# Optimization experiments

Hardware: AMD Instinct MI355X
Metric: run time of the kernel (lower is better)

The kernel has to match this reference:

```python
import jax, jax.numpy as jnp
import numpy as np

N_NODES = 100000
N_EDGES = 1600000
FEAT = 512
CLS = 64
HID = 200  # each hop layer output width; 3 hops -> 600 concat


def spmm(row, col, vals, x):
    # out[r] = sum_{e: row[e]==r} vals[e] * x[col[e]]  -- sparse A @ x
    return jax.ops.segment_sum(x[col] * vals[:, None], row, num_segments=x.shape[0])


def setup_inputs() -> dict:
    key = jax.random.key(0)
    ks = jax.random.split(key, 12)
    adj_index = jax.random.randint(ks[0], (2, N_EDGES), 0, N_NODES, dtype=jnp.int64)
    # scale like a normalized adjacency (~1/avg_degree) to keep powers stable
    adj_values = jax.random.uniform(ks[1], (N_EDGES,), dtype=jnp.float32) * (1.0 / 16.0)
    features = jax.random.normal(ks[2], (N_NODES, FEAT), dtype=jnp.float32)
    s1 = (2.0 / (FEAT + HID)) ** 0.5
    s2 = (2.0 / (3 * HID + HID)) ** 0.5
    sf = (2.0 / (3 * HID + CLS)) ** 0.5
    W1 = jax.random.normal(ks[3], (3, FEAT, HID), dtype=jnp.float32) * s1
    b1 = jax.random.normal(ks[4], (3, HID), dtype=jnp.float32) * 0.01
    W2 = jax.random.normal(ks[5], (3, 3 * HID, HID), dtype=jnp.float32) * s2
    b2 = jax.random.normal(ks[6], (3, HID), dtype=jnp.float32) * 0.01
    Wfc = jax.random.normal(ks[7], (3 * HID, CLS), dtype=jnp.float32) * sf
    bfc = jax.random.normal(ks[8], (CLS,), dtype=jnp.float32) * 0.01
    return {"adj_index": adj_index, "adj_values": adj_values, "features": features,
            "W1": W1, "b1": b1, "W2": W2, "b2": b2, "Wfc": Wfc, "bfc": bfc}


def reference(adj_index, adj_values, features, W1, b1, W2, b2, Wfc, bfc):
    # Inference mode: dropout is identity.
    row, col = adj_index[0], adj_index[1]
    # upper (sparse) layers: linear + bias + relu, then (iterations-1) spmm hops
    outs1 = []
    for i in range(3):  # iterations = i + 1
        h = jax.nn.relu(features @ W1[i] + b1[i][None, :])
        for _ in range(i):
            h = spmm(row, col, adj_values, h)
        outs1.append(h)
    abstract1 = jnp.concatenate(outs1, axis=1)  # [N, 600]
    # bottom (dense) layers: linear, (iterations-1) spmm hops, then + bias
    outs2 = []
    for i in range(3):
        h = abstract1 @ W2[i]
        for _ in range(i):
            h = spmm(row, col, adj_values, h)
        h = h + b2[i][None, :]
        outs2.append(h)
    abstract2 = jnp.concatenate(outs2, axis=1)  # [N, 600]
    node_emb = abstract2 @ Wfc + bfc  # [N, CLS]
    predictions = jax.nn.log_softmax(node_emb, axis=1)
    return node_emb, predictions
```

## Files before the change

### kernel.cpp

```cpp
#include <hip/hip_runtime.h>

typedef unsigned short u16;
typedef unsigned int u32;
typedef __attribute__((ext_vector_type(8))) short short8;
typedef __attribute__((ext_vector_type(4))) float f32x4;
typedef __attribute__((ext_vector_type(4))) u32 u32x4;
typedef __attribute__((ext_vector_type(2))) u32 u32x2;

#define NN 100000
#define PAD 640

__device__ __forceinline__ float b2f(u16 u) {
    union { u32 i; float f; } v; v.i = ((u32)u) << 16; return v.f;
}
__device__ __forceinline__ u16 f2b(float f) {
    union { float f; u32 i; } v; v.f = f;
    u32 x = v.i;
    return (u16)((x + 0x7FFFu + ((x >> 16) & 1u)) >> 16);
}
__device__ __forceinline__ u32 pack2(float lo, float hi) {
    return (u32)f2b(lo) | ((u32)f2b(hi) << 16);
}
__device__ __forceinline__ float rdf(const void* p, size_t i, int f) {
    return f ? ((const float*)p)[i] : b2f(((const u16*)p)[i]);
}
__device__ __forceinline__ void gload16(const u16* g, u16* l) {
    __builtin_amdgcn_global_load_lds(
        (const __attribute__((address_space(1))) void*)g,
        (__attribute__((address_space(3))) void*)l, 16, 0, 0);
}

__global__ void probe_k(const int* __restrict__ idx,
                        const void* avals, const void* feats, const void* W1,
                        const void* b1, const void* W2, const void* b2,
                        const void* Wfc, const void* bfc,
                        int* __restrict__ flags) {
    if (blockIdx.x != 0 || threadIdx.x >= 64) return;
    int lane = threadIdx.x;
    int v0 = idx[2 * lane + 1];
    int v1 = idx[2 * (lane + 64) + 1];
    int ok = (v0 == 0 && v1 == 0);
    int allz = __all(ok);
    if (lane == 0) flags[0] = allz ? 1 : 0;
    const void* ts[8] = {avals, feats, W1, b1, W2, b2, Wfc, bfc};
    const int ns[8] = {256, 256, 256, 128, 256, 128, 256, 32};
    for (int t = 0; t < 8; ++t) {
        const u16* p = (const u16*)ts[t];
        int n = ns[t], bad = 0;
        for (int i = lane; i < n; i += 64) {
            int e = (p[2 * i] >> 7) & 0xFF;
            if (e >= 133) bad++;
        }
        for (int off = 32; off; off >>= 1) bad += __shfl_xor(bad, off, 64);
        if (lane == 0) flags[1 + t] = (bad * 8 >= n) ? 1 : 0;
    }
}

__device__ __forceinline__ int load_row(const int* idx, int E, int f, int e) {
    return f ? idx[2 * e] : idx[e];
}
__device__ __forceinline__ int load_col(const int* idx, int E, int f, int e) {
    return f ? idx[2 * E + 2 * e] : idx[E + e];
}

__global__ void featconv_k(const void* __restrict__ src, u16* __restrict__ dst,
                           const int* __restrict__ flags) {
    int i = blockIdx.x * 256 + threadIdx.x;
    if (i >= NN * 64) return;
    int f = flags[2];
    size_t b = (size_t)i * 8;
    short8 o;
    if (f) {
        const float* sf = (const float*)src + b;
        f32x4 x0 = *(const f32x4*)sf;
        f32x4 x1 = *(const f32x4*)(sf + 4);
#pragma unroll
        for (int q = 0; q < 4; ++q) {
            o[q] = (short)f2b(x0[q]);
            o[q + 4] = (short)f2b(x1[q]);
        }
    } else {
        o = *(const short8*)((const u16*)src + b);
    }
    *(short8*)(dst + b) = o;
}

__global__ void prep_k(const void* __restrict__ W1, const void* __restrict__ W2,
                       const void* __restrict__ Wfc,
                       const void* __restrict__ b1, const void* __restrict__ b2,
                       const void* __restrict__ bfc,
                       u16* __restrict__ w1t, u16* __restrict__ w2t,
                       u16* __restrict__ wfct, float* __restrict__ biasf,
                       const int* __restrict__ flags) {
    int i = blockIdx.x * 256 + threadIdx.x;
    int job = blockIdx.y;
    if (job == 0) {
        if (i >= 640 * 512) return;
        int n = i >> 9, k = i & 511;
        float v = 0.f;
        if (n < 600) {
            int ib = n / 200, c = n % 200;
            v = rdf(W1, (size_t)ib * 102400 + (size_t)k * 200 + c, flags[3]);
        }
        w1t[i] = f2b(v);
    } else if (job == 1) {
        if (i >= 640 * 640) return;
        int n = i / 640, k = i % 640;
        float v = 0.f;
        if (n < 600 && k < 600) {
            int ib = n / 200, c = n % 200;
            v = rdf(W2, (size_t)ib * 120000 + (size_t)k * 200 + c, flags[5]);
        }
        w2t[i] = f2b(v);
    } else if (job == 2) {
        if (i >= 64 * 640) return;
        int n = i / 640, k = i % 640;
        float v = 0.f;
        if (k < 600) v = rdf(Wfc, (size_t)k * 64 + n, flags[7]);
        wfct[i] = f2b(v);
    } else {
        if (i < 600) biasf[i] = rdf(b1, i, flags[4]);
        else if (i < 1200) biasf[i] = rdf(b2, i - 600, flags[6]);
        else if (i < 1264) biasf[i] = rdf(bfc, i - 1200, flags[8]);
    }
}

__device__ __forceinline__ int pad8(int c) { return (c + 7) & ~7; }

__global__ void count_k(const int* __restrict__ idx, int E, const int* __restrict__ flags,
                        int* __restrict__ counts) {
    int e = blockIdx.x * 256 + threadIdx.x;
    if (e >= E) return;
    int r = load_row(idx, E, flags[0], e);
    if ((u32)r >= NN) return;
    atomicAdd(&counts[r], 1);
}

__global__ void chunksum_k(const int* __restrict__ counts, int* __restrict__ chsum) {
    __shared__ int sm[256];
    int c = blockIdx.x, t = threadIdx.x;
    int base = c * 1024, s = 0;
    for (int i = t; i < 1024; i += 256) {
        int g = base + i;
        if (g < NN) s += pad8(counts[g]);
    }
    sm[t] = s; __syncthreads();
    for (int off = 128; off; off >>= 1) {
        if (t < off) sm[t] += sm[t + off];
        __syncthreads();
    }
    if (t == 0) chsum[c] = sm[0];
}

__global__ void chscan_k(const int* __restrict__ chsum, int nch, int* __restrict__ choff,
                         int* __restrict__ row_ptr, int E) {
    if (threadIdx.x == 0 && blockIdx.x == 0) {
        int run = 0;
        for (int c = 0; c < nch; ++c) { choff[c] = run; run += chsum[c]; }
        row_ptr[NN] = run;
    }
}

__global__ __launch_bounds__(1024) void scan_k(const int* __restrict__ counts,
                                               const int* __restrict__ choff,
                                               int* __restrict__ row_ptr,
                                               int* __restrict__ cursor) {
    __shared__ int sm[1024];
    int c = blockIdx.x, t = threadIdx.x;
    int g = c * 1024 + t;
    int v = (g < NN) ? pad8(counts[g]) : 0;
    sm[t] = v;
    __syncthreads();
    for (int off = 1; off < 1024; off <<= 1) {
        int add = (t >= off) ? sm[t - off] : 0;
        __syncthreads();
        sm[t] += add;
        __syncthreads();
    }
    if (g < NN) {
        int ex = choff[c] + sm[t] - v;
        row_ptr[g] = ex;
        cursor[g] = ex;
    }
}

__global__ void scatter_k(const int* __restrict__ idx, const void* __restrict__ avals, int E,
                          const int* __restrict__ flags, int* __restrict__ cursor,
                          int* __restrict__ edges) {
    int e = blockIdx.x * 256 + threadIdx.x;
    if (e >= E) return;
    int f = flags[0];
    int r = load_row(idx, E, f, e);
    if ((u32)r >= NN) return;
    int c = load_col(idx, E, f, e);
    if ((u32)c >= NN) c = 0;
    int p = atomicAdd(&cursor[r], 1);
    edges[2 * p] = c;
    ((float*)edges)[2 * p + 1] = rdf(avals, e, flags[1]);
}

__global__ void padfill_k(const int* __restrict__ cursor, const int* __restrict__ row_ptr,
                          int* __restrict__ edges) {
    int r = blockIdx.x * 256 + threadIdx.x;
    if (r >= NN) return;
    int p = cursor[r], e = row_ptr[r + 1];
    for (; p < e; ++p) {
        edges[2 * p] = 0;
        ((float*)edges)[2 * p + 1] = 0.f;
    }
}

__global__ __launch_bounds__(256) void gemm128_k(
    const u16* __restrict__ A, const u16* __restrict__ Bt,
    u16* __restrict__ C, float* __restrict__ Cf,
    const float* __restrict__ bias, int bias_n, int relu,
    int M, int K, int lda, int ldc) {
    __shared__ u16 As[128 * 32];
    __shared__ u16 Bs[128 * 32];
    const int tid = threadIdx.x;
    const int wave = tid >> 6, lane = tid & 63;
    const int bm = blockIdx.x * 128, bn = blockIdx.y * 128;
    const int wrow = (wave >> 1) * 64, wcol = (wave & 1) * 64;
    const int l15 = lane & 15, l4 = lane >> 4;
    f32x4 acc[4][4] = {};

    const int c0 = wave * 2;
    const int rowA0 = c0 * 16 + (lane >> 2);
    const int rowA1 = rowA0 + 16;
    const int colE = (lane & 3) * 8;
    int gr0 = bm + rowA0; if (gr0 >= M) gr0 = M - 1;
    int gr1 = bm + rowA1; if (gr1 >= M) gr1 = M - 1;
    const u16* a0p = A + (size_t)gr0 * lda + colE;
    const u16* a1p = A + (size_t)gr1 * lda + colE;
    const u16* b0p = Bt + (size_t)(bn + rowA0) * K + colE;
    const u16* b1p = Bt + (size_t)(bn + rowA1) * K + colE;
    u16* lA0 = As + c0 * 512;
    u16* lA1 = As + c0 * 512 + 512;
    u16* lB0 = Bs + c0 * 512;
    u16* lB1 = Bs + c0 * 512 + 512;

    for (int k0 = 0; k0 < K; k0 += 32) {
        __syncthreads();
        gload16(a0p + k0, lA0);
        gload16(a1p + k0, lA1);
        gload16(b0p + k0, lB0);
        gload16(b1p + k0, lB1);
        __syncthreads();
        short8 af[4], bf[4];
#pragma unroll
        for (int t = 0; t < 4; ++t) {
            af[t] = *(const short8*)&As[(wrow + t * 16 + l15) * 32 + l4 * 8];
            bf[t] = *(const short8*)&Bs[(wcol + t * 16 + l15) * 32 + l4 * 8];
        }
#pragma unroll
        for (int mi = 0; mi < 4; ++mi)
#pragma unroll
            for (int ni = 0; ni < 4; ++ni)
                acc[mi][ni] = __builtin_amdgcn_mfma_f32_16x16x32_bf16(
                    af[mi], bf[ni], acc[mi][ni], 0, 0, 0);
    }

#pragma unroll
    for (int mi = 0; mi < 4; ++mi)
#pragma unroll
        for (int ni = 0; ni < 4; ++ni)
#pragma unroll
            for (int r4 = 0; r4 < 4; ++r4) {
                int row = bm + wrow + mi * 16 + l4 * 4 + r4;
                int col = bn + wcol + ni * 16 + l15;
                if (row < M) {
                    float v = acc[mi][ni][r4];
                    if (bias && col < bias_n) v += bias[col];
                    if (relu) v = fmaxf(v, 0.0f);
                    if (C) C[(size_t)row * ldc + col] = f2b(v);
                    if (Cf) Cf[(size_t)row * ldc + col] = v;
                }
            }
}

__global__ __launch_bounds__(256) void fc64_k(
    const u16* __restrict__ A, const u16* __restrict__ Bt,
    float* __restrict__ out_ne, float* __restrict__ out_pred,
    const float* __restrict__ bias, int M, int K, int lda) {
    __shared__ __align__(16) char ldsbuf[128 * 64 * 4];
    u16* As = (u16*)ldsbuf;
    u16* Bs = (u16*)(ldsbuf + 8192);
    float* smC = (float*)ldsbuf;

    const int tid = threadIdx.x;
    const int wave = tid >> 6, lane = tid & 63;
    const int bm = blockIdx.x * 128;
    const int wrow = (wave >> 1) * 64, wcol = (wave & 1) * 32;
    const int l15 = lane & 15, l4 = lane >> 4;
    f32x4 acc[4][2] = {};

    const int colE = (lane & 3) * 8;
    int gr0 = bm + wave * 32 + (lane >> 2); if (gr0 >= M) gr0 = M - 1;
    int gr1 = bm + wave * 32 + 16 + (lane >> 2); if (gr1 >= M) gr1 = M - 1;
    const u16* a0p = A + (size_t)gr0 * lda + colE;
    const u16* a1p = A + (size_t)gr1 * lda + colE;
    const u16* bp = Bt + (size_t)(wave * 16 + (lane >> 2)) * K + colE;
    u16* lA0 = As + wave * 1024;
    u16* lA1 = As + wave * 1024 + 512;
    u16* lB = Bs + wave * 512;

    for (int k0 = 0; k0 < K; k0 += 32) {
        __syncthreads();
        gload16(a0p + k0, lA0);
        gload16(a1p + k0, lA1);
        gload16(bp + k0, lB);
        __syncthreads();
        short8 af[4], bf[2];
#pragma unroll
        for (int t = 0; t < 4; ++t)
            af[t] = *(const short8*)&As[(wrow + t * 16 + l15) * 32 + l4 * 8];
#pragma unroll
        for (int t = 0; t < 2; ++t)
            bf[t] = *(const short8*)&Bs[(wcol + t * 16 + l15) * 32 + l4 * 8];
#pragma unroll
        for (int mi = 0; mi < 4; ++mi)
#pragma unroll
            for (int ni = 0; ni < 2; ++ni)
                acc[mi][ni] = __builtin_amdgcn_mfma_f32_16x16x32_bf16(
                    af[mi], bf[ni], acc[mi][ni], 0, 0, 0);
    }

    __syncthreads();
#pragma unroll
    for (int mi = 0; mi < 4; ++mi)
#pragma unroll
        for (int ni = 0; ni < 2; ++ni)
#pragma unroll
            for (int r4 = 0; r4 < 4; ++r4) {
                int rl = wrow + mi * 16 + l4 * 4 + r4;
                int col = wcol + ni * 16 + l15;
                int row = bm + rl;
                float v = acc[mi][ni][r4] + bias[col];
                smC[rl * 64 + col] = v;
                if (row < M) out_ne[(size_t)row * 64 + col] = v;
            }
    __syncthreads();

    const int rl = tid >> 1, half = tid & 1;
    const int row = bm + rl;
    float vv[32];
#pragma unroll
    for (int k = 0; k < 32; ++k) {
        int c = half * 32 + ((k + rl) & 31);
        vv[k] = smC[rl * 64 + c];
    }
    float m = vv[0];
#pragma unroll
    for (int k = 1; k < 32; ++k) m = fmaxf(m, vv[k]);
    m = fmaxf(m, __shfl_xor(m, 1, 64));
    float s = 0.f;
#pragma unroll
    for (int k = 0; k < 32; ++k) s += expf(vv[k] - m);
    s += __shfl_xor(s, 1, 64);
    float lg = m + logf(s);
    if (row < M) {
#pragma unroll
        for (int k = 0; k < 32; ++k) {
            int c = half * 32 + ((k + rl) & 31);
            out_pred[(size_t)row * 64 + c] = vv[k] - lg;
        }
    }
}

__global__ __launch_bounds__(256) void spmm400_k(
    const int* __restrict__ row_ptr, const int* __restrict__ edges,
    const u16* __restrict__ X, u16* __restrict__ Y1, u16* __restrict__ Yt,
    const float* __restrict__ bias1) {
    int r = blockIdx.x * 4 + (threadIdx.x >> 6);
    if (r >= NN) return;
    int lane = threadIdx.x & 63;
    int s = row_ptr[r], e = row_ptr[r + 1];
    if (s < 0) s = 0;
    if (e < s) e = s;
    float a[8] = {0.f, 0.f, 0.f, 0.f, 0.f, 0.f, 0.f, 0.f};
    const bool act = lane < 50;
    const u32* xl = (const u32*)X + lane * 4;
    for (int i = s; i < e; i += 8) {
        int cc[8]; float vv[8];
#pragma unroll
        for (int j = 0; j < 4; ++j) {
            u32x4 p = *(const u32x4*)(edges + 2 * (size_t)(i + 2 * j));
            union { u32 u; float f; } w0, w1;
            cc[2 * j] = (int)p[0];     w0.u = p[1];
            cc[2 * j + 1] = (int)p[2]; w1.u = p[3];
            vv[2 * j] = w0.f; vv[2 * j + 1] = w1.f;
        }
        if (act) {
            u32x4 g[8];
#pragma unroll
            for (int j = 0; j < 8; ++j) {
                u32 c = (u32)cc[j]; if (c >= NN) c = 0;
                g[j] = *(const u32x4*)(xl + (size_t)c * 320);
            }
#pragma unroll
            for (int j = 0; j < 8; ++j) {
                float v = vv[j];
#pragma unroll
                for (int q = 0; q < 4; ++q) {
                    union { u32 i; float f; } lo, hi;
                    lo.i = g[j][q] << 16; hi.i = g[j][q] & 0xffff0000u;
                    a[2 * q] = fmaf(v, lo.f, a[2 * q]);
                    a[2 * q + 1] = fmaf(v, hi.f, a[2 * q + 1]);
                }
            }
        }
    }
    if (bias1 && lane < 25) {
#pragma unroll
        for (int q = 0; q < 8; ++q) a[q] += bias1[lane * 8 + q];
    }
    u32x4 o;
    o[0] = pack2(a[0], a[1]); o[1] = pack2(a[2], a[3]);
    o[2] = pack2(a[4], a[5]); o[3] = pack2(a[6], a[7]);
    if (lane < 25) {
        *(u32x4*)((u32*)Y1 + (size_t)r * 320 + lane * 4) = o;
    } else if (lane < 50) {
        *(u32x4*)((u32*)Yt + (size_t)r * 100 + (lane - 25) * 4) = o;
    }
}

__global__ __launch_bounds__(256) void spmm200_k(
    const int* __restrict__ row_ptr, const int* __restrict__ edges,
    const u16* __restrict__ X, int ldx,
    u16* __restrict__ Y, int ldy,
    const float* __restrict__ bias) {
    int r = blockIdx.x * 4 + (threadIdx.x >> 6);
    if (r >= NN) return;
    int lane = threadIdx.x & 63;
    int s = row_ptr[r], e = row_ptr[r + 1];
    if (s < 0) s = 0;
    if (e < s) e = s;
    float a[4] = {0.f, 0.f, 0.f, 0.f};
    const bool act = lane < 50;
    const int ldxw = ldx >> 1, ldyw = ldy >> 1;
    const u32* xl = (const u32*)X + lane * 2;
    for (int i = s; i < e; i += 8) {
        int cc[8]; float vv[8];
#pragma unroll
        for (int j = 0; j < 4; ++j) {
            u32x4 p = *(const u32x4*)(edges + 2 * (size_t)(i + 2 * j));
            union { u32 u; float f; } w0, w1;
            cc[2 * j] = (int)p[0];     w0.u = p[1];
            cc[2 * j + 1] = (int)p[2]; w1.u = p[3];
            vv[2 * j] = w0.f; vv[2 * j + 1] = w1.f;
        }
        if (act) {
            u32x2 g[8];
#pragma unroll
            for (int j = 0; j < 8; ++j) {
                u32 c = (u32)cc[j]; if (c >= NN) c = 0;
                g[j] = *(const u32x2*)(xl + (size_t)c * ldxw);
            }
#pragma unroll
            for (int j = 0; j < 8; ++j) {
                float v = vv[j];
#pragma unroll
                for (int q = 0; q < 2; ++q) {
                    union { u32 i; float f; } lo, hi;
                    lo.i = g[j][q] << 16; hi.i = g[j][q] & 0xffff0000u;
                    a[2 * q] = fmaf(v, lo.f, a[2 * q]);
                    a[2 * q + 1] = fmaf(v, hi.f, a[2 * q + 1]);
                }
            }
        }
    }
    if (bias && act) {
#pragma unroll
        for (int q = 0; q < 4; ++q) a[q] += bias[lane * 4 + q];
    }
    if (act) {
        u32x2 o;
        o[0] = pack2(a[0], a[1]); o[1] = pack2(a[2], a[3]);
        *(u32x2*)((u32*)Y + (size_t)r * ldyw + lane * 2) = o;
    }
}

__global__ void copypad_k(const u16* __restrict__ src, u16* __restrict__ dst) {
    int i = blockIdx.x * 256 + threadIdx.x;
    if (i >= NN * 120) return;
    int r = i / 120, c = i % 120;
    if (c < 100)
        ((u32*)dst)[(size_t)r * 320 + c] = ((const u32*)src)[(size_t)r * 320 + c];
    else
        ((u32*)dst)[(size_t)r * 320 + 300 + (c - 100)] = 0u;
}
__global__ void copybias_k(const u16* __restrict__ src, u16* __restrict__ dst,
                           const float* __restrict__ bias) {
    int i = blockIdx.x * 256 + threadIdx.x;
    if (i >= NN * 200) return;
    int r = i / 200, c = i % 200;
    dst[(size_t)r * 640 + c] = f2b(b2f(src[(size_t)r * 640 + c]) + bias[c]);
}

extern "C" void kernel_launch(void* const* d_in, const int* in_sizes, int n_in,
                              void* d_out, int out_size, void* d_ws, size_t ws_size,
                              hipStream_t stream) {
    const int* adj_idx = (const int*)d_in[0];
    const void* adj_vals = d_in[1];
    const void* feats = d_in[2];
    const void* W1 = d_in[3];
    const void* b1 = d_in[4];
    const void* W2 = d_in[5];
    const void* b2 = d_in[6];
    const void* Wfc = d_in[7];
    const void* bfc = d_in[8];
    const int E = in_sizes[1];
    (void)n_in; (void)out_size; (void)ws_size;

    char* ws = (char*)d_ws;
    size_t off = 0;
    auto alloc = [&](size_t b) { size_t o = off; off += (b + 255) & ~(size_t)255; return o; };
    u16* buf0 = (u16*)(ws + alloc((size_t)NN * PAD * 2));
    u16* buf1 = (u16*)(ws + alloc((size_t)NN * PAD * 2));
    u16* hop = (u16*)(ws + alloc((size_t)NN * 200 * 2));
    u16* w1t = (u16*)(ws + alloc((size_t)640 * 512 * 2));
    u16* w2t = (u16*)(ws + alloc((size_t)640 * 640 * 2));
    u16* wfct = (u16*)(ws + alloc((size_t)64 * 640 * 2));
    float* biasf = (float*)(ws + alloc(1264 * 4));
    int* counts = (int*)(ws + alloc((size_t)NN * 4));
    int* cursor = (int*)(ws + alloc((size_t)NN * 4));
    int* row_ptr = (int*)(ws + alloc((size_t)(NN + 1) * 4));
    int* chsum = (int*)(ws + alloc(4096));
    int* choff = (int*)(ws + alloc(4096));
    int* flags = (int*)(ws + alloc(256));
    int* edgesS = (int*)(ws + alloc(((size_t)E + 8 * (size_t)NN) * 8));

    u16* featsB = buf1;
    float* out_ne = (float*)d_out;
    float* out_pred = out_ne + (size_t)NN * 64;

    probe_k<<<1, 64, 0, stream>>>(adj_idx, adj_vals, feats, W1, b1, W2, b2, Wfc, bfc, flags);
    featconv_k<<<(NN * 64 + 255) / 256, 256, 0, stream>>>(feats, featsB, flags);
    dim3 gp(1600, 4);
    prep_k<<<gp, 256, 0, stream>>>(W1, W2, Wfc, b1, b2, bfc, w1t, w2t, wfct, biasf, flags);

    hipMemsetAsync(counts, 0, NN * 4, stream);
    count_k<<<(E + 255) / 256, 256, 0, stream>>>(adj_idx, E, flags, counts);
    const int NCH = (NN + 1023) / 1024;
    chunksum_k<<<NCH, 256, 0, stream>>>(counts, chsum);
    chscan_k<<<1, 64, 0, stream>>>(chsum, NCH, choff, row_ptr, E);
    scan_k<<<NCH, 1024, 0, stream>>>(counts, choff, row_ptr, cursor);
    scatter_k<<<(E + 255) / 256, 256, 0, stream>>>(adj_idx, adj_vals, E, flags, cursor, edgesS);
    padfill_k<<<(NN + 255) / 256, 256, 0, stream>>>(cursor, row_ptr, edgesS);

    dim3 g128((NN + 127) / 128, PAD / 128);
    gemm128_k<<<g128, 256, 0, stream>>>(featsB, w1t, buf0, nullptr, biasf, 600, 1, NN, 512, 512, PAD);
    copypad_k<<<(NN * 120 + 255) / 256, 256, 0, stream>>>(buf0, buf1);
    spmm400_k<<<(NN + 3) / 4, 256, 0, stream>>>(row_ptr, edgesS,
                                                buf0 + 200, buf1 + 200, hop, nullptr);
    spmm200_k<<<(NN + 3) / 4, 256, 0, stream>>>(row_ptr, edgesS,
                                                hop, 200, buf1 + 400, PAD, nullptr);
    gemm128_k<<<g128, 256, 0, stream>>>(buf1, w2t, buf0, nullptr, nullptr, 0, 0, NN, PAD, PAD, PAD);
    copybias_k<<<(NN * 200 + 255) / 256, 256, 0, stream>>>(buf0, buf1, biasf + 600);
    spmm400_k<<<(NN + 3) / 4, 256, 0, stream>>>(row_ptr, edgesS,
                                                buf0 + 200, buf1 + 200, hop, biasf + 800);
    spmm200_k<<<(NN + 3) / 4, 256, 0, stream>>>(row_ptr, edgesS,
                                                hop, 200, buf1 + 400, PAD, biasf + 1000);
    fc64_k<<<(NN + 127) / 128, 256, 0, stream>>>(buf1, wfct, out_ne, out_pred,
                                                 biasf + 1200, NN, PAD, PAD);
}
```

Baseline: 1.589 ms.

## Fold b2 hop-0 bias into FC bias and remap GEMM blocks across XCDs

Removes the copybias pass that added b2[0] to the first 200 columns of the second GEMM output and copied them into buf1. The FC kernel now reads columns below 200 straight from buf0 and the rest from buf1. The missing bias is folded into a precomputed FC bias, b2[0]·Wfc[0:200] + bfc, built by a new prep job. The GEMM also moves from a 2D grid to a 1D grid with an XCD-aware block remap, so neighbouring tiles land on the same chiplet and share L2 better. The trade-off is some rounding difference, because the bias is no longer applied before the bf16 rounding.

```diff
diff --git a/kernel.cpp b/kernel.cpp
--- a/kernel.cpp
+++ b/kernel.cpp
@@ -118,10 +118,17 @@
         float v = 0.f;
         if (k < 600) v = rdf(Wfc, (size_t)k * 64 + n, flags[7]);
         wfct[i] = f2b(v);
-    } else {
+    } else if (job == 3) {
         if (i < 600) biasf[i] = rdf(b1, i, flags[4]);
         else if (i < 1200) biasf[i] = rdf(b2, i - 600, flags[6]);
         else if (i < 1264) biasf[i] = rdf(bfc, i - 1200, flags[8]);
+    } else {
+        if (i >= 64) return;
+        int fb2 = flags[6], fwf = flags[7];
+        float s = rdf(bfc, i, flags[8]);
+        for (int k = 0; k < 200; ++k)
+            s += rdf(b2, k, fb2) * rdf(Wfc, (size_t)k * 64 + i, fwf);
+        biasf[1280 + i] = s;
     }
 }
 
@@ -219,7 +226,14 @@
     __shared__ u16 Bs[128 * 32];
     const int tid = threadIdx.x;
     const int wave = tid >> 6, lane = tid & 63;
-    const int bm = blockIdx.x * 128, bn = blockIdx.y * 128;
+
+    const int nwg = gridDim.x;
+    const int q = nwg >> 3, r8 = nwg & 7;
+    const int xcd = blockIdx.x & 7, lo = blockIdx.x >> 3;
+    const int wg = (xcd < r8 ? xcd * (q + 1) : r8 * (q + 1) + (xcd - r8) * q) + lo;
+    const int bmi = wg / 5, bni = wg - bmi * 5;
+    const int bm = bmi * 128, bn = bni * 128;
+
     const int wrow = (wave >> 1) * 64, wcol = (wave & 1) * 64;
     const int l15 = lane & 15, l4 = lane >> 4;
     f32x4 acc[4][4] = {};
@@ -279,7 +293,8 @@
 }
 
 __global__ __launch_bounds__(256) void fc64_k(
-    const u16* __restrict__ A, const u16* __restrict__ Bt,
+    const u16* __restrict__ A0, const u16* __restrict__ A1,
+    const u16* __restrict__ Bt,
     float* __restrict__ out_ne, float* __restrict__ out_pred,
     const float* __restrict__ bias, int M, int K, int lda) {
     __shared__ __align__(16) char ldsbuf[128 * 64 * 4];
@@ -297,17 +312,22 @@
     const int colE = (lane & 3) * 8;
     int gr0 = bm + wave * 32 + (lane >> 2); if (gr0 >= M) gr0 = M - 1;
     int gr1 = bm + wave * 32 + 16 + (lane >> 2); if (gr1 >= M) gr1 = M - 1;
-    const u16* a0p = A + (size_t)gr0 * lda + colE;
-    const u16* a1p = A + (size_t)gr1 * lda + colE;
+    const u16* a0p0 = A0 + (size_t)gr0 * lda + colE;
+    const u16* a0p1 = A1 + (size_t)gr0 * lda + colE;
+    const u16* a1p0 = A0 + (size_t)gr1 * lda + colE;
+    const u16* a1p1 = A1 + (size_t)gr1 * lda + colE;
     const u16* bp = Bt + (size_t)(wave * 16 + (lane >> 2)) * K + colE;
     u16* lA0 = As + wave * 1024;
     u16* lA1 = As + wave * 1024 + 512;
     u16* lB = Bs + wave * 512;
 
     for (int k0 = 0; k0 < K; k0 += 32) {
-        __syncthreads();
-        gload16(a0p + k0, lA0);
-        gload16(a1p + k0, lA1);
+        const bool in0 = (k0 + colE) < 200;
+        const u16* pa0 = in0 ? a0p0 : a0p1;
+        const u16* pa1 = in0 ? a1p0 : a1p1;
+        __syncthreads();
+        gload16(pa0 + k0, lA0);
+        gload16(pa1 + k0, lA1);
         gload16(bp + k0, lB);
         __syncthreads();
         short8 af[4], bf[2];
@@ -489,13 +509,6 @@
     else
         ((u32*)dst)[(size_t)r * 320 + 300 + (c - 100)] = 0u;
 }
-__global__ void copybias_k(const u16* __restrict__ src, u16* __restrict__ dst,
-                           const float* __restrict__ bias) {
-    int i = blockIdx.x * 256 + threadIdx.x;
-    if (i >= NN * 200) return;
-    int r = i / 200, c = i % 200;
-    dst[(size_t)r * 640 + c] = f2b(b2f(src[(size_t)r * 640 + c]) + bias[c]);
-}
 
 extern "C" void kernel_launch(void* const* d_in, const int* in_sizes, int n_in,
                               void* d_out, int out_size, void* d_ws, size_t ws_size,
@@ -521,7 +534,7 @@
     u16* w1t = (u16*)(ws + alloc((size_t)640 * 512 * 2));
     u16* w2t = (u16*)(ws + alloc((size_t)640 * 640 * 2));
     u16* wfct = (u16*)(ws + alloc((size_t)64 * 640 * 2));
-    float* biasf = (float*)(ws + alloc(1264 * 4));
+    float* biasf = (float*)(ws + alloc(1344 * 4));
     int* counts = (int*)(ws + alloc((size_t)NN * 4));
     int* cursor = (int*)(ws + alloc((size_t)NN * 4));
     int* row_ptr = (int*)(ws + alloc((size_t)(NN + 1) * 4));
@@ -536,7 +549,7 @@
 
     probe_k<<<1, 64, 0, stream>>>(adj_idx, adj_vals, feats, W1, b1, W2, b2, Wfc, bfc, flags);
     featconv_k<<<(NN * 64 + 255) / 256, 256, 0, stream>>>(feats, featsB, flags);
-    dim3 gp(1600, 4);
+    dim3 gp(1600, 5);
     prep_k<<<gp, 256, 0, stream>>>(W1, W2, Wfc, b1, b2, bfc, w1t, w2t, wfct, biasf, flags);
 
     hipMemsetAsync(counts, 0, NN * 4, stream);
@@ -548,19 +561,18 @@
     scatter_k<<<(E + 255) / 256, 256, 0, stream>>>(adj_idx, adj_vals, E, flags, cursor, edgesS);
     padfill_k<<<(NN + 255) / 256, 256, 0, stream>>>(cursor, row_ptr, edgesS);
 
-    dim3 g128((NN + 127) / 128, PAD / 128);
-    gemm128_k<<<g128, 256, 0, stream>>>(featsB, w1t, buf0, nullptr, biasf, 600, 1, NN, 512, 512, PAD);
+    const int NWG = ((NN + 127) / 128) * 5;
+    gemm128_k<<<NWG, 256, 0, stream>>>(featsB, w1t, buf0, nullptr, biasf, 600, 1, NN, 512, 512, PAD);
     copypad_k<<<(NN * 120 + 255) / 256, 256, 0, stream>>>(buf0, buf1);
     spmm400_k<<<(NN + 3) / 4, 256, 0, stream>>>(row_ptr, edgesS,
                                                 buf0 + 200, buf1 + 200, hop, nullptr);
     spmm200_k<<<(NN + 3) / 4, 256, 0, stream>>>(row_ptr, edgesS,
                                                 hop, 200, buf1 + 400, PAD, nullptr);
-    gemm128_k<<<g128, 256, 0, stream>>>(buf1, w2t, buf0, nullptr, nullptr, 0, 0, NN, PAD, PAD, PAD);
-    copybias_k<<<(NN * 200 + 255) / 256, 256, 0, stream>>>(buf0, buf1, biasf + 600);
+    gemm128_k<<<NWG, 256, 0, stream>>>(buf1, w2t, buf0, nullptr, nullptr, 0, 0, NN, PAD, PAD, PAD);
     spmm400_k<<<(NN + 3) / 4, 256, 0, stream>>>(row_ptr, edgesS,
                                                 buf0 + 200, buf1 + 200, hop, biasf + 800);
     spmm200_k<<<(NN + 3) / 4, 256, 0, stream>>>(row_ptr, edgesS,
                                                 hop, 200, buf1 + 400, PAD, biasf + 1000);
-    fc64_k<<<(NN + 127) / 128, 256, 0, stream>>>(buf1, wfct, out_ne, out_pred,
-                                                 biasf + 1200, NN, PAD, PAD);
-}
+    fc64_k<<<(NN + 127) / 128, 256, 0, stream>>>(buf0, buf1, wfct, out_ne, out_pred,
+                                                 biasf + 1280, NN, PAD, PAD);
+}
```

Result: no change. 1.566 ms (-1.4%).
